# Kernel tuning notes

Measured on AMD Instinct MI355X. Metric: run time of the kernel, lower is better.

## Reference

```python
import jax, jax.numpy as jnp
import numpy as np

B, S, D, H, NC = 128, 256, 512, 1024, 128

def setup_inputs() -> dict:
    key = jax.random.key(0)
    ks = jax.random.split(key, 12)
    x = jax.random.randint(ks[0], (B, S, 1), 0, NC + 1)
    emb = jax.random.normal(ks[1], (NC + 1, D), dtype=jnp.float32)
    emb = emb.at[0].set(0.0)  # padding_idx=0
    def w(k, shape):
        return jax.random.normal(k, shape, dtype=jnp.float32) * (1.0 / np.sqrt(shape[0]))
    return {
        "x": x, "emb": emb,
        "Wfx": w(ks[2], (D, H)), "Wfh": w(ks[3], (H, H)), "bf": jnp.zeros(H),
        "Wix": w(ks[4], (D, H)), "Wih": w(ks[5], (H, H)), "bi": jnp.zeros(H),
        "Wgx": w(ks[6], (D, H)), "Wgh": w(ks[7], (H, H)), "bg": jnp.zeros(H),
        "Wox": w(ks[8], (D, H)), "Woh": w(ks[9], (H, H)), "bo": jnp.zeros(H),
        "Wph": w(ks[10], (H, NC)), "bp": jnp.zeros(NC),
    }

def reference(x, emb, Wfx, Wfh, bf, Wix, Wih, bi, Wgx, Wgh, bg, Wox, Woh, bo, Wph, bp):
    x_in = x[..., 0].astype(jnp.int32)            # [B,S]
    xe = emb[x_in]                                # [B,S,D]
    # Pre-compute the input-side gate projections for all timesteps (one big GEMM each).
    fx = jnp.einsum('bsd,dh->sbh', xe, Wfx) + bf
    ix = jnp.einsum('bsd,dh->sbh', xe, Wix) + bi
    gx = jnp.einsum('bsd,dh->sbh', xe, Wgx) + bg
    ox = jnp.einsum('bsd,dh->sbh', xe, Wox) + bo
    reset = (x_in > 0).astype(jnp.float32).T      # [S,B]
    def step(carry, inp):
        h, C = carry
        fx_t, ix_t, gx_t, ox_t, r_t = inp
        f = jax.nn.sigmoid(fx_t + h @ Wfh)
        i = jax.nn.sigmoid(ix_t + h @ Wih)
        g = jax.nn.sigmoid(gx_t + h @ Wgh)   # note: sigmoid (as in source), not tanh
        o = jax.nn.sigmoid(ox_t + h @ Woh)
        C = (g * i + C * f) * r_t[:, None]   # zero cell state on padding tokens
        h = o * jnp.tanh(C)
        return (h, C), None
    h0 = jnp.zeros((x.shape[0], Wfh.shape[0]), dtype=jnp.float32)
    (h, _), _ = jax.lax.scan(step, (h0, h0), (fx, ix, gx, ox, reset))
    p = h @ Wph + bp
    return jax.nn.log_softmax(p, axis=1)
```

## Files before the change

### kernel.cpp

```cpp
#include <hip/hip_runtime.h>
#include <hip/hip_bf16.h>

#define BB   128
#define SS   256
#define DD   512
#define HH   1024
#define NCC  128
#define NCLS 129
#define G4   4096
#define NWG  256

typedef __attribute__((ext_vector_type(8)))  short  short8;
typedef __attribute__((ext_vector_type(16))) float  f32x16;

static __device__ __forceinline__ float sigm(float x)  { return 1.0f / (1.0f + __expf(-x)); }
static __device__ __forceinline__ float tanh_(float x) { return 1.0f - 2.0f / (__expf(2.0f * x) + 1.0f); }
static __device__ __forceinline__ unsigned short f2b(float v) {
    __hip_bfloat16 h = __float2bfloat16(v);
    return *reinterpret_cast<unsigned short*>(&h);
}
static __device__ __forceinline__ short8 ld16(const unsigned short* p) {
    return *reinterpret_cast<const short8*>(p);
}

__global__ void k_pre(unsigned short* __restrict__ hb0, int* __restrict__ flags,
                      const float* __restrict__ Wfh, const float* __restrict__ Wih,
                      const float* __restrict__ Wgh, const float* __restrict__ Woh,
                      unsigned short* __restrict__ WhT,
                      const float* __restrict__ emb,
                      const float* __restrict__ Wfx, const float* __restrict__ Wix,
                      const float* __restrict__ Wgx, const float* __restrict__ Wox,
                      const float* __restrict__ bf_, const float* __restrict__ bi_,
                      const float* __restrict__ bg_, const float* __restrict__ bo_,
                      float* __restrict__ proj) {
    __shared__ float  t[32][33];
    __shared__ float4 wxs[128][16];
    const int bid = blockIdx.x;
    if (bid < 512) {
        int i = bid * 256 + threadIdx.x;
        if (i < BB * HH) hb0[i] = 0;
        if (i < 16384) flags[i] = 0;
        return;
    }
    if (bid < 4608) {
        int b = bid - 512;
        int bx = b & 31, by = (b >> 5) & 31, g = b >> 10;
        const float* W = (g == 0) ? Wfh : (g == 1) ? Wih : (g == 2) ? Wgh : Woh;
        int h0 = bx * 32, k0 = by * 32;
        int tx = threadIdx.x & 31, ty = threadIdx.x >> 5;
        for (int r = 0; r < 4; r++) {
            int k = ty + r * 8;
            t[k][tx] = W[(size_t)(k0 + k) * HH + h0 + tx];
        }
        __syncthreads();
        for (int r = 0; r < 4; r++) {
            int hl = ty + r * 8;
            int j  = (h0 + hl) * 4 + g;
            WhT[(size_t)j * HH + k0 + tx] = f2b(t[tx][hl]);
        }
        return;
    }
    {
        int pb = bid - 4608;
        int g = pb & 3, hcol0 = (pb >> 2) * 16;
        const float* Wx = (g == 0) ? Wfx : (g == 1) ? Wix : (g == 2) ? Wgx : Wox;
        const float* bb = (g == 0) ? bf_ : (g == 1) ? bi_ : (g == 2) ? bg_ : bo_;
        for (int i = threadIdx.x; i < 2048; i += 256) {
            int d4 = i >> 4, hc = i & 15;
            const float* w = Wx + (size_t)(d4 * 4) * HH + hcol0 + hc;
            wxs[d4][hc] = make_float4(w[0], w[HH], w[2 * HH], w[3 * HH]);
        }
        __syncthreads();
        int hc = threadIdx.x & 15, c0 = threadIdx.x >> 4;
        float bias = bb[hcol0 + hc];
        for (int c = c0; c < NCLS; c += 16) {
            const float4* er = reinterpret_cast<const float4*>(emb + (size_t)c * DD);
            float acc = bias;
            #pragma unroll 8
            for (int d4 = 0; d4 < 128; d4++) {
                float4 e = er[d4];
                float4 w = wxs[d4][hc];
                acc += e.x * w.x + e.y * w.y + e.z * w.z + e.w * w.w;
            }
            proj[(size_t)c * G4 + (hcol0 + hc) * 4 + g] = acc;
        }
    }
}

#define LDAB(d, B, L) asm volatile("global_load_dwordx4 %0, %1, off offset:" L " sc0 sc1" \
                                   : "=v"(d) : "v"(B))
#define LD4(A, I) do { \
    LDAB(A[(I)+0], p, "0"); LDAB(A[(I)+1], p, "1024"); \
    LDAB(A[(I)+2], p, "2048"); LDAB(A[(I)+3], p, "3072"); p += 4096; } while (0)
#define LD16(A) do { LD4(A,0); LD4(A,4); LD4(A,8); LD4(A,12); } while (0)

#define WAITA(N, A) asm volatile("s_waitcnt vmcnt(" N ")" : \
    "+v"(A[0]),"+v"(A[1]),"+v"(A[2]),"+v"(A[3]),"+v"(A[4]),"+v"(A[5]),"+v"(A[6]),"+v"(A[7]), \
    "+v"(A[8]),"+v"(A[9]),"+v"(A[10]),"+v"(A[11]),"+v"(A[12]),"+v"(A[13]),"+v"(A[14]),"+v"(A[15]))

#define MF16(A, KB) do { \
    acc0 = __builtin_amdgcn_mfma_f32_32x32x16_bf16(A[0],  breg[(KB)+0],  acc0, 0,0,0); \
    acc1 = __builtin_amdgcn_mfma_f32_32x32x16_bf16(A[1],  breg[(KB)+1],  acc1, 0,0,0); \
    acc0 = __builtin_amdgcn_mfma_f32_32x32x16_bf16(A[2],  breg[(KB)+2],  acc0, 0,0,0); \
    acc1 = __builtin_amdgcn_mfma_f32_32x32x16_bf16(A[3],  breg[(KB)+3],  acc1, 0,0,0); \
    acc0 = __builtin_amdgcn_mfma_f32_32x32x16_bf16(A[4],  breg[(KB)+4],  acc0, 0,0,0); \
    acc1 = __builtin_amdgcn_mfma_f32_32x32x16_bf16(A[5],  breg[(KB)+5],  acc1, 0,0,0); \
    acc0 = __builtin_amdgcn_mfma_f32_32x32x16_bf16(A[6],  breg[(KB)+6],  acc0, 0,0,0); \
    acc1 = __builtin_amdgcn_mfma_f32_32x32x16_bf16(A[7],  breg[(KB)+7],  acc1, 0,0,0); \
    acc0 = __builtin_amdgcn_mfma_f32_32x32x16_bf16(A[8],  breg[(KB)+8],  acc0, 0,0,0); \
    acc1 = __builtin_amdgcn_mfma_f32_32x32x16_bf16(A[9],  breg[(KB)+9],  acc1, 0,0,0); \
    acc0 = __builtin_amdgcn_mfma_f32_32x32x16_bf16(A[10], breg[(KB)+10], acc0, 0,0,0); \
    acc1 = __builtin_amdgcn_mfma_f32_32x32x16_bf16(A[11], breg[(KB)+11], acc1, 0,0,0); \
    acc0 = __builtin_amdgcn_mfma_f32_32x32x16_bf16(A[12], breg[(KB)+12], acc0, 0,0,0); \
    acc1 = __builtin_amdgcn_mfma_f32_32x32x16_bf16(A[13], breg[(KB)+13], acc1, 0,0,0); \
    acc0 = __builtin_amdgcn_mfma_f32_32x32x16_bf16(A[14], breg[(KB)+14], acc0, 0,0,0); \
    acc1 = __builtin_amdgcn_mfma_f32_32x32x16_bf16(A[15], breg[(KB)+15], acc1, 0,0,0); \
} while (0)

#define PRLOAD(DSTA, CLSBUF) do { \
    _Pragma("unroll") \
    for (int r = 0; r < 16; r++) { \
        int row = (r & 3) + 8 * (r >> 2) + 4 * half; \
        const float* pa = proj + (size_t)CLSBUF[row] * G4 + jg; \
        asm volatile("global_load_dword %0, %1, off" : "=v"(DSTA[r]) \
                     : "v"((unsigned long long)pa)); \
    } \
} while (0)

__global__ __launch_bounds__(128, 1)
void k_scan(const int* __restrict__ x, const float* __restrict__ proj,
            const unsigned short* __restrict__ WhT,
            unsigned short* __restrict__ hb0, unsigned short* __restrict__ hb1,
            float* __restrict__ hf32, int* __restrict__ flags) {
    const int wg = blockIdx.x, tid = threadIdx.x;
    const int lane = tid & 63, wv = tid >> 6;
    const int l31 = lane & 31, half = lane >> 5;
    const int mg = wg & 3, ng = wg >> 2;
    const int m0 = mg * 32, n0 = ng * 64;
    const int jg = n0 + wv * 32 + l31;

    short8 breg[64];
    {
        const unsigned short* Bp = WhT + (size_t)jg * HH + half * 8;
        #pragma unroll
        for (int kk = 0; kk < 64; kk++) breg[kk] = ld16(Bp + kk * 16);
    }

    __shared__ float sg[32][68];
    __shared__ int   clsW[2][2][32];

    float Cst[4] = {0.0f, 0.0f, 0.0f, 0.0f};
    const int urow = tid & 31, uq = tid >> 5;

    if (lane < 32) clsW[wv][0][lane] = x[(size_t)(m0 + lane) * SS];

    const unsigned long long ab0 =
        (unsigned long long)((char*)hb0 + mg * 65536 + lane * 16);
    const unsigned long long ab1 =
        (unsigned long long)((char*)hb1 + mg * 65536 + lane * 16);
    const unsigned long long sb0 = (unsigned long long)((char*)hb0 + mg * 65536
        + ng * 1024 + (urow + ((uq >> 1) << 5)) * 16 + (uq & 1) * 8);
    const unsigned long long sb1 = (unsigned long long)((char*)hb1 + mg * 65536
        + ng * 1024 + (urow + ((uq >> 1) << 5)) * 16 + (uq & 1) * 8);

    const unsigned long long ctrAddr =
        (unsigned long long)(flags + (size_t)(8192 + mg * 256 + (ng & 7) * 32));
    const unsigned long long pollAddr =
        (unsigned long long)(flags + (size_t)(8192 + mg * 256 + (lane & 7) * 32));

    float pr[16];
    PRLOAD(pr, clsW[wv][0]);

    for (int s = 0; s < SS; s++) {
        const int cur = s & 1;
        unsigned long long p = cur ? ab1 : ab0;
        const unsigned long long sb = cur ? sb0 : sb1;

        short8 a0[16], a1[16], a2[16], a3[16];
        LD16(a0);
        LD16(a1);

        f32x16 acc0, acc1;
        #pragma unroll
        for (int r = 0; r < 16; r++) { acc0[r] = 0.0f; acc1[r] = 0.0f; }

        WAITA("16", a0);
        LD16(a2);
        MF16(a0, 0);
        WAITA("16", a1);
        LD16(a3);
        MF16(a1, 16);
        WAITA("16", a2);
        MF16(a2, 32);
        WAITA("0", a3);
        MF16(a3, 48);

        #pragma unroll
        for (int r = 0; r < 16; r++) {
            int row = (r & 3) + 8 * (r >> 2) + 4 * half;
            sg[row][wv * 32 + l31] = sigm(acc0[r] + acc1[r] + pr[r]);
        }
        asm volatile("s_waitcnt lgkmcnt(0)" ::: "memory");

        {
            const float rr = (clsW[wv][cur][urow] > 0) ? 1.0f : 0.0f;
            unsigned short hv[4];
            #pragma unroll
            for (int q = 0; q < 4; q++) {
                float4 gq = *reinterpret_cast<const float4*>(&sg[urow][uq * 16 + q * 4]);
                float cn = (gq.z * gq.y + Cst[q] * gq.x) * rr;
                Cst[q] = cn;
                float hvv = gq.w * tanh_(cn);
                hv[q] = f2b(hvv);
                if (s == SS - 1)
                    hf32[(size_t)(m0 + urow) * HH + ng * 16 + uq * 4 + q] = hvv;
            }
            unsigned long long pk = (unsigned long long)hv[0]
                                  | ((unsigned long long)hv[1] << 16)
                                  | ((unsigned long long)hv[2] << 32)
                                  | ((unsigned long long)hv[3] << 48);
            asm volatile("global_store_dwordx2 %0, %1, off sc0 sc1" :: "v"(sb), "v"(pk) : "memory");
            if (s + 1 < SS && lane < 32)
                clsW[wv][cur ^ 1][lane] = x[(size_t)(m0 + lane) * SS + s + 1];
        }

        if (s < SS - 1) {
            asm volatile("s_waitcnt vmcnt(0)" ::: "memory");
            if (lane == 0) {
                int one = 1;
                asm volatile("global_atomic_add %0, %1, off"
                             :: "v"(ctrAddr), "v"(one) : "memory");
            }
            PRLOAD(pr, clsW[wv][cur ^ 1]);
            const int tv = (s + 1) << 4;
            int got;
            do {
                asm volatile("global_load_dword %0, %1, off sc0 sc1\n\t"
                             "s_waitcnt vmcnt(0)"
                             : "=v"(got) : "v"(pollAddr) : "memory");
            } while (__ballot(got >= tv) != ~0ull);
        }
    }
}

__global__ void k_final(const float* __restrict__ hf32, const float* __restrict__ Wph,
                        const float* __restrict__ bp, float* __restrict__ out) {
    __shared__ float part[512];
    __shared__ float red[128];
    const int b = blockIdx.x, tid = threadIdx.x;
    const int c = tid & 127, q = tid >> 7;
    const float* hr = hf32 + (size_t)b * HH + q * 256;
    const float* wp = Wph + (size_t)(q * 256) * NCC + c;
    float acc = 0.0f;
    #pragma unroll 8
    for (int k = 0; k < 256; k++) acc += hr[k] * wp[(size_t)k * NCC];
    part[tid] = acc;
    __syncthreads();
    float a = 0.0f;
    if (tid < 128) {
        a = part[c] + part[c + 128] + part[c + 256] + part[c + 384] + bp[c];
        red[c] = a;
    }
    __syncthreads();
    for (int st = 64; st > 0; st >>= 1) {
        if (tid < st) red[tid] = fmaxf(red[tid], red[tid + st]);
        __syncthreads();
    }
    float m = red[0];
    __syncthreads();
    if (tid < 128) red[tid] = __expf(a - m);
    __syncthreads();
    for (int st = 64; st > 0; st >>= 1) {
        if (tid < st) red[tid] += red[tid + st];
        __syncthreads();
    }
    if (tid < 128) out[(size_t)b * NCC + tid] = a - m - __logf(red[0]);
}

extern "C" void kernel_launch(void* const* d_in, const int* in_sizes, int n_in,
                              void* d_out, int out_size, void* d_ws, size_t ws_size,
                              hipStream_t stream) {
    const int*   x   = (const int*)  d_in[0];
    const float* emb = (const float*)d_in[1];
    const float* Wfx = (const float*)d_in[2];
    const float* Wfh = (const float*)d_in[3];
    const float* bf_ = (const float*)d_in[4];
    const float* Wix = (const float*)d_in[5];
    const float* Wih = (const float*)d_in[6];
    const float* bi_ = (const float*)d_in[7];
    const float* Wgx = (const float*)d_in[8];
    const float* Wgh = (const float*)d_in[9];
    const float* bg_ = (const float*)d_in[10];
    const float* Wox = (const float*)d_in[11];
    const float* Woh = (const float*)d_in[12];
    const float* bo_ = (const float*)d_in[13];
    const float* Wph = (const float*)d_in[14];
    const float* bp_ = (const float*)d_in[15];
    float* out = (float*)d_out;

    char* ws = (char*)d_ws;
    unsigned short* WhT   = (unsigned short*)(ws);
    float*          proj  = (float*)(ws + 8388608);
    int*            flags = (int*)(ws + 10502656);
    unsigned short* hb0   = (unsigned short*)(ws + 10568192);
    unsigned short* hb1   = (unsigned short*)(ws + 10830336);
    float*          hf32  = (float*)(ws + 11092480);

    k_pre<<<dim3(4864), dim3(256), 0, stream>>>(hb0, flags, Wfh, Wih, Wgh, Woh, WhT,
                                                emb, Wfx, Wix, Wgx, Wox,
                                                bf_, bi_, bg_, bo_, proj);
    k_scan<<<dim3(NWG), dim3(128), 0, stream>>>(x, proj, WhT, hb0, hb1, hf32, flags);
    k_final<<<dim3(128), dim3(512), 0, stream>>>(hf32, Wph, bp_, out);
}
```

Measured before the change: 1.278 ms.

## Fuse preprocessing, recurrent scan and output head into one persistent kernel

Merges the weight transpose/bf16 conversion, the embedding-projection table, the LSTM scan and the final log-softmax head into a single persistent kernel of 256 workgroups. Grid-wide barriers built on the existing atomic counters separate the phases, and the flag reset moves to a memset. The aim is to remove two kernel launches and their gaps. In exchange, preprocessing now runs on only 256 small workgroups instead of thousands, and the final head uses just 128 of them.

Measured after the change: 1.286 ms. Within noise of the previous version (+0.6%).

```diff
diff --git a/kernel.cpp b/kernel.cpp
--- a/kernel.cpp
+++ b/kernel.cpp
@@ -21,70 +21,6 @@
 }
 static __device__ __forceinline__ short8 ld16(const unsigned short* p) {
     return *reinterpret_cast<const short8*>(p);
-}
-
-__global__ void k_pre(unsigned short* __restrict__ hb0, int* __restrict__ flags,
-                      const float* __restrict__ Wfh, const float* __restrict__ Wih,
-                      const float* __restrict__ Wgh, const float* __restrict__ Woh,
-                      unsigned short* __restrict__ WhT,
-                      const float* __restrict__ emb,
-                      const float* __restrict__ Wfx, const float* __restrict__ Wix,
-                      const float* __restrict__ Wgx, const float* __restrict__ Wox,
-                      const float* __restrict__ bf_, const float* __restrict__ bi_,
-                      const float* __restrict__ bg_, const float* __restrict__ bo_,
-                      float* __restrict__ proj) {
-    __shared__ float  t[32][33];
-    __shared__ float4 wxs[128][16];
-    const int bid = blockIdx.x;
-    if (bid < 512) {
-        int i = bid * 256 + threadIdx.x;
-        if (i < BB * HH) hb0[i] = 0;
-        if (i < 16384) flags[i] = 0;
-        return;
-    }
-    if (bid < 4608) {
-        int b = bid - 512;
-        int bx = b & 31, by = (b >> 5) & 31, g = b >> 10;
-        const float* W = (g == 0) ? Wfh : (g == 1) ? Wih : (g == 2) ? Wgh : Woh;
-        int h0 = bx * 32, k0 = by * 32;
-        int tx = threadIdx.x & 31, ty = threadIdx.x >> 5;
-        for (int r = 0; r < 4; r++) {
-            int k = ty + r * 8;
-            t[k][tx] = W[(size_t)(k0 + k) * HH + h0 + tx];
-        }
-        __syncthreads();
-        for (int r = 0; r < 4; r++) {
-            int hl = ty + r * 8;
-            int j  = (h0 + hl) * 4 + g;
-            WhT[(size_t)j * HH + k0 + tx] = f2b(t[tx][hl]);
-        }
-        return;
-    }
-    {
-        int pb = bid - 4608;
-        int g = pb & 3, hcol0 = (pb >> 2) * 16;
-        const float* Wx = (g == 0) ? Wfx : (g == 1) ? Wix : (g == 2) ? Wgx : Wox;
-        const float* bb = (g == 0) ? bf_ : (g == 1) ? bi_ : (g == 2) ? bg_ : bo_;
-        for (int i = threadIdx.x; i < 2048; i += 256) {
-            int d4 = i >> 4, hc = i & 15;
-            const float* w = Wx + (size_t)(d4 * 4) * HH + hcol0 + hc;
-            wxs[d4][hc] = make_float4(w[0], w[HH], w[2 * HH], w[3 * HH]);
-        }
-        __syncthreads();
-        int hc = threadIdx.x & 15, c0 = threadIdx.x >> 4;
-        float bias = bb[hcol0 + hc];
-        for (int c = c0; c < NCLS; c += 16) {
-            const float4* er = reinterpret_cast<const float4*>(emb + (size_t)c * DD);
-            float acc = bias;
-            #pragma unroll 8
-            for (int d4 = 0; d4 < 128; d4++) {
-                float4 e = er[d4];
-                float4 w = wxs[d4][hc];
-                acc += e.x * w.x + e.y * w.y + e.z * w.z + e.w * w.w;
-            }
-            proj[(size_t)c * G4 + (hcol0 + hc) * 4 + g] = acc;
-        }
-    }
 }
 
 #define LDAB(d, B, L) asm volatile("global_load_dwordx4 %0, %1, off offset:" L " sc0 sc1" \
@@ -128,10 +64,18 @@
 } while (0)
 
 __global__ __launch_bounds__(128, 1)
-void k_scan(const int* __restrict__ x, const float* __restrict__ proj,
-            const unsigned short* __restrict__ WhT,
-            unsigned short* __restrict__ hb0, unsigned short* __restrict__ hb1,
-            float* __restrict__ hf32, int* __restrict__ flags) {
+void k_all(const int* __restrict__ x, const float* __restrict__ emb,
+           const float* __restrict__ Wfh, const float* __restrict__ Wih,
+           const float* __restrict__ Wgh, const float* __restrict__ Woh,
+           const float* __restrict__ Wfx, const float* __restrict__ Wix,
+           const float* __restrict__ Wgx, const float* __restrict__ Wox,
+           const float* __restrict__ bf_, const float* __restrict__ bi_,
+           const float* __restrict__ bg_, const float* __restrict__ bo_,
+           const float* __restrict__ Wph, const float* __restrict__ bp,
+           unsigned short* __restrict__ WhT, float* __restrict__ proj,
+           unsigned short* __restrict__ hb0, unsigned short* __restrict__ hb1,
+           float* __restrict__ hf32, int* __restrict__ flags,
+           float* __restrict__ out) {
     const int wg = blockIdx.x, tid = threadIdx.x;
     const int lane = tid & 63, wv = tid >> 6;
     const int l31 = lane & 31, half = lane >> 5;
@@ -139,15 +83,94 @@
     const int m0 = mg * 32, n0 = ng * 64;
     const int jg = n0 + wv * 32 + l31;
 
+    __shared__ float  tls[32][33];
+    __shared__ float4 wxs[128][16];
+    __shared__ float  sg[32][68];
+    __shared__ int    clsW[2][2][32];
+    __shared__ float  red[128];
+
+    const unsigned long long ctrAddr =
+        (unsigned long long)(flags + (size_t)(8192 + mg * 256 + (ng & 7) * 32));
+    const unsigned long long pollAddr =
+        (unsigned long long)(flags + (size_t)(8192 + mg * 256 + (lane & 7) * 32));
+    const unsigned long long gpollAddr =
+        (unsigned long long)(flags + (size_t)(8192 + ((lane >> 3) & 3) * 256 + (lane & 7) * 32));
+
+    {
+        unsigned long long za =
+            (unsigned long long)((char*)hb0 + ((size_t)wg * 128 + tid) * 8);
+        unsigned long long z64 = 0;
+        asm volatile("global_store_dwordx2 %0, %1, off sc0 sc1" :: "v"(za), "v"(z64) : "memory");
+    }
+    for (int t = 0; t < 16; t++) {
+        int b = wg * 16 + t;
+        int bx = b & 31, by = (b >> 5) & 31, g = b >> 10;
+        const float* W = (g == 0) ? Wfh : (g == 1) ? Wih : (g == 2) ? Wgh : Woh;
+        int h0 = bx * 32, k0 = by * 32;
+        int tx = tid & 31, ty = tid >> 5;
+        for (int r = 0; r < 8; r++) {
+            int k = ty + r * 4;
+            tls[k][tx] = W[(size_t)(k0 + k) * HH + h0 + tx];
+        }
+        __syncthreads();
+        for (int r = 0; r < 8; r++) {
+            int hl = ty + r * 4;
+            int j  = (h0 + hl) * 4 + g;
+            int v  = (int)f2b(tls[tx][hl]);
+            unsigned long long wa =
+                (unsigned long long)(WhT + (size_t)j * HH + k0 + tx);
+            asm volatile("global_store_short %0, %1, off sc0 sc1" :: "v"(wa), "v"(v) : "memory");
+        }
+        __syncthreads();
+    }
+    {
+        int g = wg & 3, hcol0 = (wg >> 2) * 16;
+        const float* Wx = (g == 0) ? Wfx : (g == 1) ? Wix : (g == 2) ? Wgx : Wox;
+        const float* bb = (g == 0) ? bf_ : (g == 1) ? bi_ : (g == 2) ? bg_ : bo_;
+        for (int i = tid; i < 2048; i += 128) {
+            int d4 = i >> 4, hc = i & 15;
+            const float* w = Wx + (size_t)(d4 * 4) * HH + hcol0 + hc;
+            wxs[d4][hc] = make_float4(w[0], w[HH], w[2 * HH], w[3 * HH]);
+        }
+        __syncthreads();
+        int hc = tid & 15, c0 = tid >> 4;
+        float bias = bb[hcol0 + hc];
+        for (int c = c0; c < NCLS; c += 8) {
+            const float4* er = reinterpret_cast<const float4*>(emb + (size_t)c * DD);
+            float acc = bias;
+            #pragma unroll 8
+            for (int d4 = 0; d4 < 128; d4++) {
+                float4 e = er[d4];
+                float4 w = wxs[d4][hc];
+                acc += e.x * w.x + e.y * w.y + e.z * w.z + e.w * w.w;
+            }
+            unsigned long long pa = (unsigned long long)
+                (proj + (size_t)c * G4 + (hcol0 + hc) * 4 + g);
+            asm volatile("global_store_dword %0, %1, off sc0 sc1" :: "v"(pa), "v"(acc) : "memory");
+        }
+    }
+    asm volatile("s_waitcnt vmcnt(0)" ::: "memory");
+    __syncthreads();
+    if (lane == 0) {
+        int one = 1;
+        asm volatile("global_atomic_add %0, %1, off" :: "v"(ctrAddr), "v"(one) : "memory");
+    }
+    {
+        int got;
+        do {
+            asm volatile("global_load_dword %0, %1, off sc0 sc1\n\t"
+                         "s_waitcnt vmcnt(0)"
+                         : "=v"(got) : "v"(gpollAddr) : "memory");
+        } while (__ballot(got >= 16) != ~0ull);
+    }
+    __builtin_amdgcn_fence(__ATOMIC_ACQUIRE, "agent");
+
     short8 breg[64];
     {
         const unsigned short* Bp = WhT + (size_t)jg * HH + half * 8;
         #pragma unroll
         for (int kk = 0; kk < 64; kk++) breg[kk] = ld16(Bp + kk * 16);
     }
-
-    __shared__ float sg[32][68];
-    __shared__ int   clsW[2][2][32];
 
     float Cst[4] = {0.0f, 0.0f, 0.0f, 0.0f};
     const int urow = tid & 31, uq = tid >> 5;
@@ -162,11 +185,6 @@
         + ng * 1024 + (urow + ((uq >> 1) << 5)) * 16 + (uq & 1) * 8);
     const unsigned long long sb1 = (unsigned long long)((char*)hb1 + mg * 65536
         + ng * 1024 + (urow + ((uq >> 1) << 5)) * 16 + (uq & 1) * 8);
-
-    const unsigned long long ctrAddr =
-        (unsigned long long)(flags + (size_t)(8192 + mg * 256 + (ng & 7) * 32));
-    const unsigned long long pollAddr =
-        (unsigned long long)(flags + (size_t)(8192 + mg * 256 + (lane & 7) * 32));
 
     float pr[16];
     PRLOAD(pr, clsW[wv][0]);
@@ -212,8 +230,12 @@
                 Cst[q] = cn;
                 float hvv = gq.w * tanh_(cn);
                 hv[q] = f2b(hvv);
-                if (s == SS - 1)
-                    hf32[(size_t)(m0 + urow) * HH + ng * 16 + uq * 4 + q] = hvv;
+                if (s == SS - 1) {
+                    unsigned long long ha = (unsigned long long)
+                        (hf32 + (size_t)(m0 + urow) * HH + ng * 16 + uq * 4 + q);
+                    asm volatile("global_store_dword %0, %1, off sc0 sc1"
+                                 :: "v"(ha), "v"(hvv) : "memory");
+                }
             }
             unsigned long long pk = (unsigned long long)hv[0]
                                   | ((unsigned long long)hv[1] << 16)
@@ -232,7 +254,7 @@
                              :: "v"(ctrAddr), "v"(one) : "memory");
             }
             PRLOAD(pr, clsW[wv][cur ^ 1]);
-            const int tv = (s + 1) << 4;
+            const int tv = (s + 2) << 4;
             int got;
             do {
                 asm volatile("global_load_dword %0, %1, off sc0 sc1\n\t"
@@ -241,40 +263,51 @@
             } while (__ballot(got >= tv) != ~0ull);
         }
     }
-}
-
-__global__ void k_final(const float* __restrict__ hf32, const float* __restrict__ Wph,
-                        const float* __restrict__ bp, float* __restrict__ out) {
-    __shared__ float part[512];
-    __shared__ float red[128];
-    const int b = blockIdx.x, tid = threadIdx.x;
-    const int c = tid & 127, q = tid >> 7;
-    const float* hr = hf32 + (size_t)b * HH + q * 256;
-    const float* wp = Wph + (size_t)(q * 256) * NCC + c;
-    float acc = 0.0f;
-    #pragma unroll 8
-    for (int k = 0; k < 256; k++) acc += hr[k] * wp[(size_t)k * NCC];
-    part[tid] = acc;
-    __syncthreads();
-    float a = 0.0f;
-    if (tid < 128) {
-        a = part[c] + part[c + 128] + part[c + 256] + part[c + 384] + bp[c];
-        red[c] = a;
-    }
-    __syncthreads();
-    for (int st = 64; st > 0; st >>= 1) {
-        if (tid < st) red[tid] = fmaxf(red[tid], red[tid + st]);
-        __syncthreads();
-    }
-    float m = red[0];
-    __syncthreads();
-    if (tid < 128) red[tid] = __expf(a - m);
-    __syncthreads();
-    for (int st = 64; st > 0; st >>= 1) {
-        if (tid < st) red[tid] += red[tid + st];
-        __syncthreads();
-    }
-    if (tid < 128) out[(size_t)b * NCC + tid] = a - m - __logf(red[0]);
+
+    asm volatile("s_waitcnt vmcnt(0)" ::: "memory");
+    if (lane == 0) {
+        int one = 1;
+        asm volatile("global_atomic_add %0, %1, off" :: "v"(ctrAddr), "v"(one) : "memory");
+    }
+    {
+        const int tv = (SS + 1) << 4;
+        int got;
+        do {
+            asm volatile("global_load_dword %0, %1, off sc0 sc1\n\t"
+                         "s_waitcnt vmcnt(0)"
+                         : "=v"(got) : "v"(gpollAddr) : "memory");
+        } while (__ballot(got >= tv) != ~0ull);
+    }
+    __builtin_amdgcn_fence(__ATOMIC_ACQUIRE, "agent");
+
+    if (wg < BB) {
+        const int b = wg, c = tid;
+        const float* hr = hf32 + (size_t)b * HH;
+        const float* wp = Wph + c;
+        float acc = bp[c];
+        const float4* h4 = reinterpret_cast<const float4*>(hr);
+        #pragma unroll 8
+        for (int k4 = 0; k4 < 256; k4++) {
+            float4 h = h4[k4];
+            const float* w = wp + (size_t)(k4 * 4) * NCC;
+            acc += h.x * w[0] + h.y * w[NCC] + h.z * w[2 * NCC] + h.w * w[3 * NCC];
+        }
+        red[c] = acc;
+        __syncthreads();
+        for (int st = 64; st > 0; st >>= 1) {
+            if (c < st) red[c] = fmaxf(red[c], red[c + st]);
+            __syncthreads();
+        }
+        float m = red[0];
+        __syncthreads();
+        red[c] = __expf(acc - m);
+        __syncthreads();
+        for (int st = 64; st > 0; st >>= 1) {
+            if (c < st) red[c] += red[c + st];
+            __syncthreads();
+        }
+        out[(size_t)b * NCC + c] = acc - m - __logf(red[0]);
+    }
 }
 
 extern "C" void kernel_launch(void* const* d_in, const int* in_sizes, int n_in,
@@ -306,9 +339,9 @@
     unsigned short* hb1   = (unsigned short*)(ws + 10830336);
     float*          hf32  = (float*)(ws + 11092480);
 
-    k_pre<<<dim3(4864), dim3(256), 0, stream>>>(hb0, flags, Wfh, Wih, Wgh, Woh, WhT,
-                                                emb, Wfx, Wix, Wgx, Wox,
-                                                bf_, bi_, bg_, bo_, proj);
-    k_scan<<<dim3(NWG), dim3(128), 0, stream>>>(x, proj, WhT, hb0, hb1, hf32, flags);
-    k_final<<<dim3(128), dim3(512), 0, stream>>>(hf32, Wph, bp_, out);
+    hipMemsetAsync(flags, 0, 16384 * sizeof(int), stream);
+    k_all<<<dim3(NWG), dim3(128), 0, stream>>>(
+        x, emb, Wfh, Wih, Wgh, Woh, Wfx, Wix, Wgx, Wox,
+        bf_, bi_, bg_, bo_, Wph, bp_,
+        WhT, proj, hb0, hb1, hf32, flags, out);
 }
```
